# Optimization experiments

Hardware: AMD Instinct MI355X
Metric: run time of the kernel (lower is better)

The kernel has to match this reference:

```python
import jax, jax.numpy as jnp
import numpy as np

T = 3000
D_MODEL = 1280
NUM_HEADS = 20
HEAD_DIM = D_MODEL // NUM_HEADS
N_CHUNKS = 4  # block-diagonal chunks of 750 frames each
NEG = -1e9


def _block_diag_mask(t, n_chunks):
    chunk = t // n_chunks
    seg = jnp.arange(t) // chunk  # [T]
    allow = seg[:, None] == seg[None, :]
    return jnp.where(allow, 0.0, NEG).astype(jnp.float32)


def setup_inputs() -> dict:
    key = jax.random.key(0)
    ks = jax.random.split(key, 9)
    s = 1.0 / np.sqrt(D_MODEL)
    inp = {
        "hidden_states": jax.random.normal(ks[0], (T, D_MODEL), jnp.float32),
        "attention_mask": _block_diag_mask(T, N_CHUNKS),
        "wq": jax.random.normal(ks[1], (D_MODEL, D_MODEL), jnp.float32) * s,
        "bq": jax.random.normal(ks[2], (D_MODEL,), jnp.float32) * 0.02,
        "wk": jax.random.normal(ks[3], (D_MODEL, D_MODEL), jnp.float32) * s,
        "bk": jax.random.normal(ks[4], (D_MODEL,), jnp.float32) * 0.02,
        "wv": jax.random.normal(ks[5], (D_MODEL, D_MODEL), jnp.float32) * s,
        "bv": jax.random.normal(ks[6], (D_MODEL,), jnp.float32) * 0.02,
        "wo": jax.random.normal(ks[7], (D_MODEL, D_MODEL), jnp.float32) * s,
        "bo": jax.random.normal(ks[8], (D_MODEL,), jnp.float32) * 0.02,
    }
    return inp


def reference(hidden_states, attention_mask, wq, bq, wk, bk, wv, bv, wo, bo):
    # hidden_states: [T, D], attention_mask: [T, T] additive (0 / -inf)
    t = hidden_states.shape[0]
    scaling = HEAD_DIM ** -0.5
    # projections -> [H, T, hd]  (weights stored as [in, out] = W^T of nn.Linear)
    q = (hidden_states @ wq + bq).reshape(t, NUM_HEADS, HEAD_DIM).transpose(1, 0, 2)
    k = (hidden_states @ wk + bk).reshape(t, NUM_HEADS, HEAD_DIM).transpose(1, 0, 2)
    v = (hidden_states @ wv + bv).reshape(t, NUM_HEADS, HEAD_DIM).transpose(1, 0, 2)
    # [H, T, T] scores + additive mask, fp32 softmax
    scores = jnp.einsum("htd,hsd->hts", q, k) * scaling + attention_mask[None]
    attn = jax.nn.softmax(scores.astype(jnp.float32), axis=-1).astype(q.dtype)
    out = jnp.einsum("hts,hsd->htd", attn, v)  # [H, T, hd]
    out = out.transpose(1, 0, 2).reshape(t, D_MODEL)
    return out @ wo + bo
```

## Files before the change

### kernel.cpp

```cpp
#include <hip/hip_runtime.h>

#define T_LEN 3000
#define DM 1280
#define NUM_HEADS 20
#define N_CH 4
#define CHUNK 750
#define CHUNK_PAD 768
#define T_PAD 3072

typedef __bf16 bf16x8 __attribute__((ext_vector_type(8)));
typedef float f32x4 __attribute__((ext_vector_type(4)));
typedef float f32x16 __attribute__((ext_vector_type(16)));

typedef const __attribute__((address_space(1))) void* gas_p;
typedef __attribute__((address_space(3))) void* las_p;
#define GLOAD16(g, l) __builtin_amdgcn_global_load_lds((gas_p)(g), (las_p)(l), 16, 0, 0)

#define LOG2E 1.44269504088896340736f

__device__ __forceinline__ unsigned short f2bf(float f) {
  __bf16 b = (__bf16)f;
  union { __bf16 b; unsigned short u; } x; x.b = b;
  return x.u;
}

#define NB_CVT (T_PAD * DM / 4 / 256)
#define NB_TR  (40 * 40 * 4)
__global__ __launch_bounds__(256) void prep_kernel(
    const float* __restrict__ hs, unsigned short* __restrict__ Xb,
    const float* __restrict__ w0, const float* __restrict__ w1,
    const float* __restrict__ w2, const float* __restrict__ w3,
    unsigned short* __restrict__ Wcat, unsigned short* __restrict__ Vtb) {
  const int b = blockIdx.x;
  if (b < NB_CVT) {
    int i = b * 256 + threadIdx.x;
    ushort4 o;
    if (i < T_LEN * DM / 4) {
      const float4 v = ((const float4*)hs)[i];
      o.x = f2bf(v.x); o.y = f2bf(v.y); o.z = f2bf(v.z); o.w = f2bf(v.w);
    } else {
      o.x = 0; o.y = 0; o.z = 0; o.w = 0;
    }
    ((ushort4*)Xb)[i] = o;
    return;
  }
  if (b < NB_CVT + NB_TR) {
    const int bb = b - NB_CVT;
    const int z = bb / 1600;
    const int rem = bb - z * 1600;
    const int bx = rem % 40, by = rem / 40;
    const float* in = z == 0 ? w0 : (z == 1 ? w1 : (z == 2 ? w2 : w3));
    unsigned short* o = Wcat + (size_t)z * DM * DM;
    __shared__ float tile[32][33];
    const int x = threadIdx.x & 31, y0 = threadIdx.x >> 5;
    const int n0 = bx * 32, k0 = by * 32;
    for (int y = y0; y < 32; y += 8) tile[y][x] = in[(k0 + y) * DM + n0 + x];
    __syncthreads();
    for (int y = y0; y < 32; y += 8) o[(n0 + y) * DM + k0 + x] = f2bf(tile[x][y]);
    return;
  }
  for (int i = threadIdx.x; i < NUM_HEADS * 64 * N_CH * (CHUNK_PAD - CHUNK); i += 256) {
    int c = i % (CHUNK_PAD - CHUNK); int r = i / (CHUNK_PAD - CHUNK);
    int ch = r % N_CH; int row = r / N_CH;
    Vtb[(size_t)row * T_PAD + ch * CHUNK_PAD + CHUNK + c] = 0;
  }
}

__global__ __launch_bounds__(256) void gemm_qkv_kernel(
    const unsigned short* __restrict__ A, const unsigned short* __restrict__ Bt,
    const float* __restrict__ b0, const float* __restrict__ b1, const float* __restrict__ b2,
    unsigned short* __restrict__ dq, unsigned short* __restrict__ dk,
    unsigned short* __restrict__ dv) {
  __shared__ unsigned short As[128][64];
  __shared__ unsigned short Bs[128][64];
  const int tid = threadIdx.x;
  const int lane = tid & 63, wave = tid >> 6;
  const int h = lane >> 4, lr = lane & 15;
  const int wm = wave >> 1, wn = wave & 1;
  const int t0 = blockIdx.x * 128, n0 = blockIdx.y * 128;
  const int rs = lane >> 3;
  const int c8 = (lane & 7) ^ rs;

  const unsigned short* Ab = A + (size_t)t0 * DM + c8 * 8;
  const unsigned short* Bb = Bt + (size_t)n0 * DM + c8 * 8;

  f32x4 acc[4][4];
  const f32x4 zero4 = {0.f, 0.f, 0.f, 0.f};
#pragma unroll
  for (int i = 0; i < 4; i++)
#pragma unroll
    for (int j = 0; j < 4; j++) acc[i][j] = zero4;

  const int NT = DM / 64;
  for (int kt = 0; kt < NT; ++kt) {
    const int k0 = kt * 64;
#pragma unroll
    for (int i = 0; i < 4; ++i) {
      const int blk = wave * 4 + i;
      const size_t ro = (size_t)(blk * 8 + rs) * DM + k0;
      GLOAD16(Ab + ro, &As[blk * 8][0]);
      GLOAD16(Bb + ro, &Bs[blk * 8][0]);
    }
    __syncthreads();
#pragma unroll
    for (int kk = 0; kk < 2; ++kk) {
      bf16x8 a[4], b[4];
      const int csw = ((kk * 4 + h) ^ (lr & 7)) * 8;
#pragma unroll
      for (int mi = 0; mi < 4; mi++) a[mi] = *(const bf16x8*)&As[wm * 64 + mi * 16 + lr][csw];
#pragma unroll
      for (int ni = 0; ni < 4; ni++) b[ni] = *(const bf16x8*)&Bs[wn * 64 + ni * 16 + lr][csw];
#pragma unroll
      for (int mi = 0; mi < 4; mi++)
#pragma unroll
        for (int ni = 0; ni < 4; ni++)
          acc[mi][ni] = __builtin_amdgcn_mfma_f32_16x16x32_bf16(a[mi], b[ni], acc[mi][ni], 0, 0, 0);
    }
    __syncthreads();
  }

  const int sec = (int)blockIdx.y / 10;
  const float* bias = sec == 0 ? b0 : (sec == 1 ? b1 : b2);
  const float qs = sec == 0 ? (0.125f * LOG2E) : 1.0f;
#pragma unroll
  for (int mi = 0; mi < 4; mi++) {
#pragma unroll
    for (int j = 0; j < 4; j++) {
      int t = t0 + wm * 64 + mi * 16 + h * 4 + j;
      if (t >= T_LEN) continue;
#pragma unroll
      for (int ni = 0; ni < 4; ni++) {
        int n = n0 + wn * 64 + ni * 16 + lr;
        int nn = n - sec * DM;
        float v = (acc[mi][ni][j] + bias[nn]) * qs;
        if (sec < 2) {
          unsigned short* dst = sec == 0 ? dq : dk;
          dst[(size_t)(nn >> 6) * (T_PAD * 64) + (size_t)t * 64 + (nn & 63)] = f2bf(v);
        } else {
          int ch = t / CHUNK, s = t - ch * CHUNK;
          dv[(size_t)(nn >> 6) * (64 * T_PAD) + (size_t)(nn & 63) * T_PAD + ch * CHUNK_PAD + s] = f2bf(v);
        }
      }
    }
  }
}

__global__ __launch_bounds__(256) void gemm_out_kernel(
    const unsigned short* __restrict__ A, const unsigned short* __restrict__ Bt,
    const float* __restrict__ b0, float* __restrict__ df) {
  __shared__ unsigned short As[64][64];
  __shared__ unsigned short Bs[64][64];
  const int tid = threadIdx.x;
  const int lane = tid & 63, wave = tid >> 6;
  const int h = lane >> 4, lr = lane & 15;
  const int wm = wave >> 1, wn = wave & 1;
  const int t0 = blockIdx.x * 64, n0 = blockIdx.y * 64;
  const int rs = lane >> 3;
  const int c8 = (lane & 7) ^ rs;

  const unsigned short* Ab = A + (size_t)t0 * DM + c8 * 8;
  const unsigned short* Bb = Bt + (size_t)n0 * DM + c8 * 8;

  f32x4 acc[2][2];
  const f32x4 zero4 = {0.f, 0.f, 0.f, 0.f};
#pragma unroll
  for (int i = 0; i < 2; i++)
#pragma unroll
    for (int j = 0; j < 2; j++) acc[i][j] = zero4;

  const int NT = DM / 64;
  for (int kt = 0; kt < NT; ++kt) {
    const int k0 = kt * 64;
#pragma unroll
    for (int i = 0; i < 2; ++i) {
      const int blk = wave * 2 + i;
      const size_t ro = (size_t)(blk * 8 + rs) * DM + k0;
      GLOAD16(Ab + ro, &As[blk * 8][0]);
      GLOAD16(Bb + ro, &Bs[blk * 8][0]);
    }
    __syncthreads();
#pragma unroll
    for (int kk = 0; kk < 2; ++kk) {
      bf16x8 a[2], b[2];
      const int csw = ((kk * 4 + h) ^ (lr & 7)) * 8;
#pragma unroll
      for (int mi = 0; mi < 2; mi++) a[mi] = *(const bf16x8*)&As[wm * 32 + mi * 16 + lr][csw];
#pragma unroll
      for (int ni = 0; ni < 2; ni++) b[ni] = *(const bf16x8*)&Bs[wn * 32 + ni * 16 + lr][csw];
#pragma unroll
      for (int mi = 0; mi < 2; mi++)
#pragma unroll
        for (int ni = 0; ni < 2; ni++)
          acc[mi][ni] = __builtin_amdgcn_mfma_f32_16x16x32_bf16(a[mi], b[ni], acc[mi][ni], 0, 0, 0);
    }
    __syncthreads();
  }

#pragma unroll
  for (int mi = 0; mi < 2; mi++) {
#pragma unroll
    for (int j = 0; j < 4; j++) {
      int t = t0 + wm * 32 + mi * 16 + h * 4 + j;
      if (t >= T_LEN) continue;
#pragma unroll
      for (int ni = 0; ni < 2; ni++) {
        int n = n0 + wn * 32 + ni * 16 + lr;
        df[(size_t)t * DM + n] = acc[mi][ni][j] + b0[n];
      }
    }
  }
}

__global__ __launch_bounds__(128) void attn_kernel(
    const unsigned short* __restrict__ Qb, const unsigned short* __restrict__ Kb,
    const unsigned short* __restrict__ Vtb, unsigned short* __restrict__ Ctx) {
  __shared__ unsigned short Ks[2][64][64];
  __shared__ unsigned short Vs[2][64][64];
  __shared__ unsigned short Ps[2][32][64];
  const int tid = threadIdx.x;
  const int lane = tid & 63, wave = tid >> 6;
  const int l31 = lane & 31, hi = lane >> 5;
  const int rs = lane >> 3;
  const int c8s = (lane & 7) ^ rs;
  int bid = blockIdx.x;
  const int qt = bid % 12; bid /= 12;
  const int ch = bid % N_CH; bid /= N_CH;
  const int hh = bid;

  const unsigned short* Qh = Qb + (size_t)hh * (T_PAD * 64);
  const unsigned short* Kh = Kb + (size_t)hh * (T_PAD * 64) + (size_t)(ch * CHUNK) * 64 + c8s * 8;
  const unsigned short* Vh = Vtb + (size_t)hh * (64 * T_PAD) + ch * CHUNK_PAD + c8s * 8;

  const int qrow0 = qt * 64 + wave * 32;
  const int tq = ch * CHUNK + qrow0 + l31;
  bf16x8 aq[4];
#pragma unroll
  for (int s = 0; s < 4; s++)
    aq[s] = *(const bf16x8*)(Qh + (size_t)tq * 64 + s * 16 + hi * 8);

  f32x16 oacc0, oacc1;
#pragma unroll
  for (int i = 0; i < 16; i++) { oacc0[i] = 0.f; oacc1[i] = 0.f; }
  float l_part[16];
#pragma unroll
  for (int i = 0; i < 16; i++) l_part[i] = 0.f;

#define A_STAGE(buf, kt) do {                                                   \
    const int s0_ = (kt) * 64;                                                  \
    _Pragma("unroll")                                                           \
    for (int i_ = 0; i_ < 4; ++i_) {                                            \
      const int blk_ = wave * 4 + i_;                                           \
      const int r_ = blk_ * 8 + rs;                                             \
      GLOAD16(Kh + (size_t)(s0_ + r_) * 64, &Ks[buf][blk_ * 8][0]);             \
      GLOAD16(Vh + (size_t)r_ * T_PAD + s0_, &Vs[buf][blk_ * 8][0]);            \
    } } while (0)

  A_STAGE(0, 0);
  __syncthreads();
  int cur = 0;
  const int xk = l31 & 7;
  for (int kt = 0; kt < 12; ++kt) {
    if (kt + 1 < 12) A_STAGE(cur ^ 1, kt + 1);

    f32x16 s0, s1;
#pragma unroll
    for (int i = 0; i < 16; i++) { s0[i] = 0.f; s1[i] = 0.f; }
    __builtin_amdgcn_s_setprio(1);
#pragma unroll
    for (int s = 0; s < 4; s++) {
      const int cx = ((2 * s + hi) ^ xk) * 8;
      bf16x8 k0 = *(const bf16x8*)&Ks[cur][l31][cx];
      bf16x8 k1 = *(const bf16x8*)&Ks[cur][32 + l31][cx];
      s0 = __builtin_amdgcn_mfma_f32_32x32x16_bf16(aq[s], k0, s0, 0, 0, 0);
      s1 = __builtin_amdgcn_mfma_f32_32x32x16_bf16(aq[s], k1, s1, 0, 0, 0);
    }
    __builtin_amdgcn_s_setprio(0);

    const bool lastt = (kt == 11);
#pragma unroll
    for (int r = 0; r < 16; r++) {
      float e0 = exp2f(s0[r]);
      float e1 = exp2f(s1[r]);
      if (lastt && (l31 >= 14)) e1 = 0.f;
      l_part[r] += e0 + e1;
      const int row = (r & 3) + 8 * (r >> 2) + 4 * hi;
      const int r7 = (r & 3) + 4 * hi;
      Ps[wave][row][(((l31 >> 3) ^ r7) << 3) + (l31 & 7)] = f2bf(e0);
      Ps[wave][row][((((l31 >> 3) + 4) ^ r7) << 3) + (l31 & 7)] = f2bf(e1);
    }

    __builtin_amdgcn_s_setprio(1);
#pragma unroll
    for (int s = 0; s < 4; s++) {
      const int cx = ((2 * s + hi) ^ xk) * 8;
      bf16x8 pa = *(const bf16x8*)&Ps[wave][l31][cx];
      bf16x8 v0 = *(const bf16x8*)&Vs[cur][l31][cx];
      bf16x8 v1 = *(const bf16x8*)&Vs[cur][32 + l31][cx];
      oacc0 = __builtin_amdgcn_mfma_f32_32x32x16_bf16(pa, v0, oacc0, 0, 0, 0);
      oacc1 = __builtin_amdgcn_mfma_f32_32x32x16_bf16(pa, v1, oacc1, 0, 0, 0);
    }
    __builtin_amdgcn_s_setprio(0);
    __syncthreads();
    cur ^= 1;
  }
#undef A_STAGE

#pragma unroll
  for (int r = 0; r < 16; r++) {
    float l = l_part[r];
#pragma unroll
    for (int off = 1; off < 32; off <<= 1) l += __shfl_xor(l, off, 64);
    l_part[r] = 1.f / l;
  }
#pragma unroll
  for (int r = 0; r < 16; r++) {
    const int row = (r & 3) + 8 * (r >> 2) + 4 * hi;
    int qr = qrow0 + row;
    if (qr >= CHUNK) continue;
    int t = ch * CHUNK + qr;
    Ctx[(size_t)t * DM + hh * 64 + l31] = f2bf(oacc0[r] * l_part[r]);
    Ctx[(size_t)t * DM + hh * 64 + 32 + l31] = f2bf(oacc1[r] * l_part[r]);
  }
}

extern "C" void kernel_launch(void* const* d_in, const int* in_sizes, int n_in,
                              void* d_out, int out_size, void* d_ws, size_t ws_size,
                              hipStream_t stream) {
  const float* hs = (const float*)d_in[0];
  const float* wq = (const float*)d_in[2];
  const float* bq = (const float*)d_in[3];
  const float* wk = (const float*)d_in[4];
  const float* bk = (const float*)d_in[5];
  const float* wv = (const float*)d_in[6];
  const float* bv = (const float*)d_in[7];
  const float* wo = (const float*)d_in[8];
  const float* bo = (const float*)d_in[9];

  char* ws = (char*)d_ws;
  unsigned short* Xb = (unsigned short*)ws;   ws += (size_t)T_PAD * DM * 2;
  unsigned short* Wcat = (unsigned short*)ws; ws += (size_t)4 * DM * DM * 2;
  unsigned short* Qb = (unsigned short*)ws;   ws += (size_t)NUM_HEADS * T_PAD * 64 * 2;
  unsigned short* Kb = (unsigned short*)ws;   ws += (size_t)NUM_HEADS * T_PAD * 64 * 2;
  unsigned short* Vtb = (unsigned short*)ws;  ws += (size_t)NUM_HEADS * 64 * T_PAD * 2;
  unsigned short* Ctx = (unsigned short*)ws;  ws += (size_t)T_PAD * DM * 2;

  prep_kernel<<<NB_CVT + NB_TR + 1, 256, 0, stream>>>(hs, Xb, wq, wk, wv, wo, Wcat, Vtb);

  gemm_qkv_kernel<<<dim3(24, 30), 256, 0, stream>>>(Xb, Wcat, bq, bk, bv, Qb, Kb, Vtb);

  attn_kernel<<<NUM_HEADS * N_CH * 12, 128, 0, stream>>>(Qb, Kb, Vtb, Ctx);

  gemm_out_kernel<<<dim3(48, 20), 256, 0, stream>>>(Ctx, Wcat + (size_t)3 * DM * DM, bo, (float*)d_out);
}
```

Before: 133.1 us.

## Replace QKV and output GEMMs with single-wave double-buffered 64x64 GEMM kernel

Both projection GEMMs now use one templated kernel in which each 64-thread block (a single wave) computes a 64x64 tile with a K-step of 32. Shared-memory tiles are double-buffered and the next stage is prefetched with explicit vmcnt waits instead of block-wide barriers. The QKV grid grows to 48x60 small blocks and the output GEMM gets 4x4 MFMA tiles per wave. This removes __syncthreads and adds load/compute overlap, at the cost of less data reuse per block, more global traffic from smaller tiles, and correctness that depends on the inline waitcnt ordering.

```diff
diff --git a/kernel.cpp b/kernel.cpp
--- a/kernel.cpp
+++ b/kernel.cpp
@@ -66,23 +66,22 @@
   }
 }
 
-__global__ __launch_bounds__(256) void gemm_qkv_kernel(
+template <int MODE>
+__global__ __launch_bounds__(64) void gemm1w_kernel(
     const unsigned short* __restrict__ A, const unsigned short* __restrict__ Bt,
     const float* __restrict__ b0, const float* __restrict__ b1, const float* __restrict__ b2,
     unsigned short* __restrict__ dq, unsigned short* __restrict__ dk,
-    unsigned short* __restrict__ dv) {
-  __shared__ unsigned short As[128][64];
-  __shared__ unsigned short Bs[128][64];
-  const int tid = threadIdx.x;
-  const int lane = tid & 63, wave = tid >> 6;
+    unsigned short* __restrict__ dv, float* __restrict__ df) {
+  __shared__ unsigned short As[2][64][32];
+  __shared__ unsigned short Bs[2][64][32];
+  const int lane = threadIdx.x;
   const int h = lane >> 4, lr = lane & 15;
-  const int wm = wave >> 1, wn = wave & 1;
-  const int t0 = blockIdx.x * 128, n0 = blockIdx.y * 128;
-  const int rs = lane >> 3;
-  const int c8 = (lane & 7) ^ rs;
-
-  const unsigned short* Ab = A + (size_t)t0 * DM + c8 * 8;
-  const unsigned short* Bb = Bt + (size_t)n0 * DM + c8 * 8;
+  const int t0 = blockIdx.x * 64, n0 = blockIdx.y * 64;
+
+  const int srow = lane >> 2;
+  const int c4 = (lane & 3) ^ (srow & 3);
+  const unsigned short* Aln = A + (size_t)(t0 + srow) * DM + c4 * 8;
+  const unsigned short* Bln = Bt + (size_t)(n0 + srow) * DM + c4 * 8;
 
   f32x4 acc[4][4];
   const f32x4 zero4 = {0.f, 0.f, 0.f, 0.f};
@@ -91,121 +90,71 @@
 #pragma unroll
     for (int j = 0; j < 4; j++) acc[i][j] = zero4;
 
-  const int NT = DM / 64;
-  for (int kt = 0; kt < NT; ++kt) {
-    const int k0 = kt * 64;
-#pragma unroll
-    for (int i = 0; i < 4; ++i) {
-      const int blk = wave * 4 + i;
-      const size_t ro = (size_t)(blk * 8 + rs) * DM + k0;
-      GLOAD16(Ab + ro, &As[blk * 8][0]);
-      GLOAD16(Bb + ro, &Bs[blk * 8][0]);
-    }
-    __syncthreads();
-#pragma unroll
-    for (int kk = 0; kk < 2; ++kk) {
-      bf16x8 a[4], b[4];
-      const int csw = ((kk * 4 + h) ^ (lr & 7)) * 8;
-#pragma unroll
-      for (int mi = 0; mi < 4; mi++) a[mi] = *(const bf16x8*)&As[wm * 64 + mi * 16 + lr][csw];
-#pragma unroll
-      for (int ni = 0; ni < 4; ni++) b[ni] = *(const bf16x8*)&Bs[wn * 64 + ni * 16 + lr][csw];
-#pragma unroll
-      for (int mi = 0; mi < 4; mi++)
-#pragma unroll
-        for (int ni = 0; ni < 4; ni++)
-          acc[mi][ni] = __builtin_amdgcn_mfma_f32_16x16x32_bf16(a[mi], b[ni], acc[mi][ni], 0, 0, 0);
-    }
-    __syncthreads();
-  }
-
-  const int sec = (int)blockIdx.y / 10;
-  const float* bias = sec == 0 ? b0 : (sec == 1 ? b1 : b2);
-  const float qs = sec == 0 ? (0.125f * LOG2E) : 1.0f;
+  const int NT = DM / 32;
+
+#define G_STAGE(SL, kt) do {                                                  \
+    const size_t ko_ = (size_t)(kt) * 32;                                     \
+    _Pragma("unroll")                                                         \
+    for (int g_ = 0; g_ < 4; ++g_) {                                          \
+      GLOAD16(Aln + (size_t)(g_ * 16) * DM + ko_, &As[SL][g_ * 16][0]);       \
+      GLOAD16(Bln + (size_t)(g_ * 16) * DM + ko_, &Bs[SL][g_ * 16][0]);       \
+    } } while (0)
+
+#define K_STEP(kt, SL) do {                                                   \
+    asm volatile("s_waitcnt lgkmcnt(0)" ::: "memory");                        \
+    if ((kt) + 1 < NT) {                                                      \
+      G_STAGE(SL ^ 1, (kt) + 1);                                              \
+      asm volatile("s_waitcnt vmcnt(8)" ::: "memory");                        \
+    } else {                                                                  \
+      asm volatile("s_waitcnt vmcnt(0)" ::: "memory");                        \
+    }                                                                         \
+    bf16x8 a[4], b[4];                                                        \
+    const int cx_ = (h ^ (lr & 3)) * 8;                                       \
+    _Pragma("unroll")                                                         \
+    for (int mi = 0; mi < 4; mi++) a[mi] = *(const bf16x8*)&As[SL][mi * 16 + lr][cx_]; \
+    _Pragma("unroll")                                                         \
+    for (int ni = 0; ni < 4; ni++) b[ni] = *(const bf16x8*)&Bs[SL][ni * 16 + lr][cx_]; \
+    _Pragma("unroll")                                                         \
+    for (int mi = 0; mi < 4; mi++)                                            \
+      _Pragma("unroll")                                                       \
+      for (int ni = 0; ni < 4; ni++)                                          \
+        acc[mi][ni] = __builtin_amdgcn_mfma_f32_16x16x32_bf16(a[mi], b[ni], acc[mi][ni], 0, 0, 0); \
+  } while (0)
+
+  G_STAGE(0, 0);
+#pragma unroll 1
+  for (int kt = 0; kt < NT; kt += 2) {
+    K_STEP(kt, 0);
+    K_STEP(kt + 1, 1);
+  }
+#undef K_STEP
+#undef G_STAGE
+
+  const int sec = (MODE == 0) ? ((int)blockIdx.y / 20) : 0;
+  const float* bias = (MODE == 0) ? (sec == 0 ? b0 : (sec == 1 ? b1 : b2)) : b0;
+  const float qs = (MODE == 0 && sec == 0) ? (0.125f * LOG2E) : 1.0f;
 #pragma unroll
   for (int mi = 0; mi < 4; mi++) {
 #pragma unroll
     for (int j = 0; j < 4; j++) {
-      int t = t0 + wm * 64 + mi * 16 + h * 4 + j;
+      int t = t0 + mi * 16 + h * 4 + j;
       if (t >= T_LEN) continue;
 #pragma unroll
       for (int ni = 0; ni < 4; ni++) {
-        int n = n0 + wn * 64 + ni * 16 + lr;
-        int nn = n - sec * DM;
-        float v = (acc[mi][ni][j] + bias[nn]) * qs;
-        if (sec < 2) {
-          unsigned short* dst = sec == 0 ? dq : dk;
-          dst[(size_t)(nn >> 6) * (T_PAD * 64) + (size_t)t * 64 + (nn & 63)] = f2bf(v);
+        int n = n0 + ni * 16 + lr;
+        if (MODE == 0) {
+          int nn = n - sec * DM;
+          float v = (acc[mi][ni][j] + bias[nn]) * qs;
+          if (sec < 2) {
+            unsigned short* dst = sec == 0 ? dq : dk;
+            dst[(size_t)(nn >> 6) * (T_PAD * 64) + (size_t)t * 64 + (nn & 63)] = f2bf(v);
+          } else {
+            int ch = t / CHUNK, s = t - ch * CHUNK;
+            dv[(size_t)(nn >> 6) * (64 * T_PAD) + (size_t)(nn & 63) * T_PAD + ch * CHUNK_PAD + s] = f2bf(v);
+          }
         } else {
-          int ch = t / CHUNK, s = t - ch * CHUNK;
-          dv[(size_t)(nn >> 6) * (64 * T_PAD) + (size_t)(nn & 63) * T_PAD + ch * CHUNK_PAD + s] = f2bf(v);
+          df[(size_t)t * DM + n] = acc[mi][ni][j] + b0[n];
         }
-      }
-    }
-  }
-}
-
-__global__ __launch_bounds__(256) void gemm_out_kernel(
-    const unsigned short* __restrict__ A, const unsigned short* __restrict__ Bt,
-    const float* __restrict__ b0, float* __restrict__ df) {
-  __shared__ unsigned short As[64][64];
-  __shared__ unsigned short Bs[64][64];
-  const int tid = threadIdx.x;
-  const int lane = tid & 63, wave = tid >> 6;
-  const int h = lane >> 4, lr = lane & 15;
-  const int wm = wave >> 1, wn = wave & 1;
-  const int t0 = blockIdx.x * 64, n0 = blockIdx.y * 64;
-  const int rs = lane >> 3;
-  const int c8 = (lane & 7) ^ rs;
-
-  const unsigned short* Ab = A + (size_t)t0 * DM + c8 * 8;
-  const unsigned short* Bb = Bt + (size_t)n0 * DM + c8 * 8;
-
-  f32x4 acc[2][2];
-  const f32x4 zero4 = {0.f, 0.f, 0.f, 0.f};
-#pragma unroll
-  for (int i = 0; i < 2; i++)
-#pragma unroll
-    for (int j = 0; j < 2; j++) acc[i][j] = zero4;
-
-  const int NT = DM / 64;
-  for (int kt = 0; kt < NT; ++kt) {
-    const int k0 = kt * 64;
-#pragma unroll
-    for (int i = 0; i < 2; ++i) {
-      const int blk = wave * 2 + i;
-      const size_t ro = (size_t)(blk * 8 + rs) * DM + k0;
-      GLOAD16(Ab + ro, &As[blk * 8][0]);
-      GLOAD16(Bb + ro, &Bs[blk * 8][0]);
-    }
-    __syncthreads();
-#pragma unroll
-    for (int kk = 0; kk < 2; ++kk) {
-      bf16x8 a[2], b[2];
-      const int csw = ((kk * 4 + h) ^ (lr & 7)) * 8;
-#pragma unroll
-      for (int mi = 0; mi < 2; mi++) a[mi] = *(const bf16x8*)&As[wm * 32 + mi * 16 + lr][csw];
-#pragma unroll
-      for (int ni = 0; ni < 2; ni++) b[ni] = *(const bf16x8*)&Bs[wn * 32 + ni * 16 + lr][csw];
-#pragma unroll
-      for (int mi = 0; mi < 2; mi++)
-#pragma unroll
-        for (int ni = 0; ni < 2; ni++)
-          acc[mi][ni] = __builtin_amdgcn_mfma_f32_16x16x32_bf16(a[mi], b[ni], acc[mi][ni], 0, 0, 0);
-    }
-    __syncthreads();
-  }
-
-#pragma unroll
-  for (int mi = 0; mi < 2; mi++) {
-#pragma unroll
-    for (int j = 0; j < 4; j++) {
-      int t = t0 + wm * 32 + mi * 16 + h * 4 + j;
-      if (t >= T_LEN) continue;
-#pragma unroll
-      for (int ni = 0; ni < 2; ni++) {
-        int n = n0 + wn * 32 + ni * 16 + lr;
-        df[(size_t)t * DM + n] = acc[mi][ni][j] + b0[n];
       }
     }
   }
@@ -346,9 +295,10 @@
 
   prep_kernel<<<NB_CVT + NB_TR + 1, 256, 0, stream>>>(hs, Xb, wq, wk, wv, wo, Wcat, Vtb);
 
-  gemm_qkv_kernel<<<dim3(24, 30), 256, 0, stream>>>(Xb, Wcat, bq, bk, bv, Qb, Kb, Vtb);
+  gemm1w_kernel<0><<<dim3(48, 60), 64, 0, stream>>>(Xb, Wcat, bq, bk, bv, Qb, Kb, Vtb, nullptr);
 
   attn_kernel<<<NUM_HEADS * N_CH * 12, 128, 0, stream>>>(Qb, Kb, Vtb, Ctx);
 
-  gemm_out_kernel<<<dim3(48, 20), 256, 0, stream>>>(Ctx, Wcat + (size_t)3 * DM * DM, bo, (float*)d_out);
-}
+  gemm1w_kernel<1><<<dim3(48, 20), 64, 0, stream>>>(Ctx, Wcat + (size_t)3 * DM * DM, bo, nullptr, nullptr,
+                                                    nullptr, nullptr, nullptr, (float*)d_out);
+}
```

Result: slower. 182.2 us (+36.9%).
